# Kernel tuning notes

Measured on AMD Instinct MI355X. Metric: run time of the kernel, lower is better.

Reference implementation:

```python
import jax, jax.numpy as jnp
import numpy as np

C = 16; HP = 16; WP = 16; D = 32; KITER = 4; P = 8; N = P * P; B = 16; HID = 64


def conv2d(x, w, b):
    # x: (B, Cin, H, W), w: (Cout, Cin, kh, kw), 'same' padding for 3x3
    y = jax.lax.conv_general_dilated(x, w, (1, 1), [(1, 1), (1, 1)],
                                     dimension_numbers=('NCHW', 'OIHW', 'NCHW'))
    return y + b[None, :, None, None]


def setup_inputs() -> dict:
    key = jax.random.key(0)
    ks = jax.random.split(key, 20)
    n = lambda k, shape, s=0.1: jax.random.normal(k, shape, jnp.float32) * s
    # 4-neighbor directed grid edges over P x P nodes
    edges = []
    for p in range(P):
        for q in range(P):
            i = p * P + q
            for dp, dq in ((0, 1), (1, 0), (0, -1), (-1, 0)):
                pp, qq = p + dp, q + dq
                if 0 <= pp < P and 0 <= qq < P:
                    edges.append((i, pp * P + qq))
    edge_index = jnp.asarray(np.asarray(edges, np.int32))  # (E, 2) with (i=dst, j=src)
    return {
        'seed': n(ks[0], (B, C, P * HP, P * WP), 1.0),
        'edge_index': edge_index,
        'wq': n(ks[1], (C, D)), 'bq': jnp.zeros((D,), jnp.float32),
        'wk': n(ks[2], (C, D)), 'bk': jnp.zeros((D,), jnp.float32),
        'wm': n(ks[3], (C, C, 3, 3)), 'bm': jnp.zeros((C,), jnp.float32),
        'a_w1': n(ks[4], (2 * D, HID)), 'a_b1': jnp.zeros((HID,), jnp.float32),
        'a_w2': n(ks[5], (HID, HID)), 'a_b2': jnp.zeros((HID,), jnp.float32),
        'a_wo': n(ks[6], (HID, 1)), 'a_bo': jnp.zeros((1,), jnp.float32),
        'g_w': n(ks[7], (C, 1, 3, 3)), 'g_b': jnp.zeros((C,), jnp.float32),
        'gru_wg': n(ks[8], (2 * C, 2 * C, 3, 3)), 'gru_bg': jnp.zeros((2 * C,), jnp.float32),
        'gru_wc': n(ks[9], (C, 2 * C, 3, 3)), 'gru_bc': jnp.zeros((C,), jnp.float32),
    }


def reference(seed, edge_index, wq, bq, wk, bk, wm, bm,
              a_w1, a_b1, a_w2, a_b2, a_wo, a_bo,
              g_w, g_b, gru_wg, gru_bg, gru_wc, gru_bc):
    Bb, Cc, PH, PW = seed.shape
    Pp = PH // HP
    Nn = Pp * Pp
    # patchify: (B,C,PH,PW) -> (B,N,C,H,W), node order is row-major (p,q)
    X = seed.reshape(Bb, Cc, Pp, HP, Pp, WP).transpose(0, 2, 4, 1, 3, 5).reshape(Bb, Nn, Cc, HP, WP)
    ei = edge_index[:, 0]  # dst node i
    ej = edge_index[:, 1]  # src node j
    # GateConv on a spatially-constant map e: conv(e*ones) = e * conv(ones) (+bias).
    ones_map = jnp.ones((1, 1, HP, WP), seed.dtype)
    T = jax.lax.conv_general_dilated(ones_map, g_w, (1, 1), [(1, 1), (1, 1)],
                                     dimension_numbers=('NCHW', 'OIHW', 'NCHW'))  # (1,C,H,W)
    for _ in range(KITER):
        xm = X.mean((-2, -1))  # (B,N,C); mean commutes with the 1x1 convs f_Q/f_K
        q_vec = xm @ wq + bq   # (B,N,d)
        k_vec = xm @ wk + bk
        M = conv2d(X.reshape(Bb * Nn, Cc, HP, WP), wm, bm).reshape(Bb, Nn, Cc, HP, WP)
        # per-edge attention scores via ConcatMLP
        h0 = jnp.concatenate([q_vec[:, ei], k_vec[:, ej]], axis=-1)  # (B,E,2d)
        h1 = jax.nn.relu(h0 @ a_w1 + a_b1)
        h2 = jax.nn.relu(h1 @ a_w2 + a_b2)
        e = (h2 @ a_wo + a_bo)[..., 0]  # (B,E)
        # gate map and gated messages
        G = jax.nn.sigmoid(e[:, :, None, None, None] * T[None] + g_b[None, None, :, None, None])  # (B,E,C,H,W)
        msg = G * M[:, ej]  # gather src patches, gate
        agg = jax.ops.segment_sum(jnp.moveaxis(msg, 1, 0), ei, num_segments=Nn)  # (N,B,C,H,W)
        M_agg = jnp.moveaxis(agg, 0, 1).reshape(Bb * Nn, Cc, HP, WP)
        # ConvGRU cell update
        h = X.reshape(Bb * Nn, Cc, HP, WP)
        zr = jax.nn.sigmoid(conv2d(jnp.concatenate([M_agg, h], axis=1), gru_wg, gru_bg))
        z, r = zr[:, :Cc], zr[:, Cc:]
        cand = jnp.tanh(conv2d(jnp.concatenate([M_agg, r * h], axis=1), gru_wc, gru_bc))
        X = ((1.0 - z) * h + z * cand).reshape(Bb, Nn, Cc, HP, WP)
    # unpatchify
    out = X.reshape(Bb, Pp, Pp, Cc, HP, WP).transpose(0, 3, 1, 4, 2, 5).reshape(Bb, Cc, PH, PW)
    return out
```

## Files before the change

### kernel.cpp

```cpp
#include <hip/hip_runtime.h>
#include <hip/hip_bf16.h>

#define Bt 16
#define Ct 16
#define Nt 64
#define KITERt 4

#define WF_TOTAL 25681
#define SWZ_TOTAL 16384
#define SETUP_IDX (WF_TOTAL + 4096 + Nt + SWZ_TOTAL)
#define SAH_STRIDE 40

typedef __attribute__((ext_vector_type(8))) short bf16x8;
typedef __attribute__((ext_vector_type(4))) short s16x4;
typedef __attribute__((ext_vector_type(4))) float f32x4;

__device__ inline float bf2f(__hip_bfloat16 v) { return __bfloat162float(v); }
__device__ inline short f2bs(float f) {
    __hip_bfloat16 h = __float2bfloat16(f);
    short s; __builtin_memcpy(&s, &h, 2); return s;
}
__device__ inline float bs2f(short s) {
    __hip_bfloat16 h; __builtin_memcpy(&h, &s, 2);
    return __bfloat162float(h);
}
__device__ inline float loadf(const void* p, int i, int isf32) {
    return isf32 ? ((const float*)p)[i]
                 : __bfloat162float(((const __hip_bfloat16*)p)[i]);
}
__device__ inline float sigm(float x) {
    return __builtin_amdgcn_rcpf(1.f + __expf(-x));
}
__device__ inline float tanh_fast(float x) {
    float e = __expf(2.f * x);
    return 1.f - 2.f * __builtin_amdgcn_rcpf(e + 1.f);
}

__global__ __launch_bounds__(256) void setup_kernel(
    const void* __restrict__ seed,
    const void* __restrict__ wq, const void* __restrict__ bq,
    const void* __restrict__ wk, const void* __restrict__ bk,
    const void* __restrict__ wm, const void* __restrict__ bm,
    const void* __restrict__ w1, const void* __restrict__ b1,
    const void* __restrict__ w2, const void* __restrict__ b2,
    const void* __restrict__ wo, const void* __restrict__ bo,
    const void* __restrict__ gw, const void* __restrict__ gb,
    const void* __restrict__ wg, const void* __restrict__ bg,
    const void* __restrict__ wc, const void* __restrict__ bc,
    const int* __restrict__ edge, int E,
    float* __restrict__ Wf, float* __restrict__ Tswz,
    int* __restrict__ counts, int* __restrict__ nbrs,
    __hip_bfloat16* __restrict__ swz,
    short* __restrict__ Xb, float* __restrict__ qv0, float* __restrict__ kv0,
    int* __restrict__ flag)
{
    __shared__ float sred[4];
    __shared__ int sflag;
    __shared__ float xred[64];
    int bn = blockIdx.x, t = threadIdx.x;
    int lane = t & 63, wv = t >> 6;

    {
        float v = fabsf(__bfloat162float(((const __hip_bfloat16*)seed)[t]));
        if (!(v <= 1e30f)) v = 1e30f;
#pragma unroll
        for (int off = 1; off < 64; off <<= 1) v = fmaxf(v, __shfl_xor(v, off, 64));
        if (lane == 0) sred[wv] = v;
        __syncthreads();
        if (t == 0) {
            float m = fmaxf(fmaxf(sred[0], sred[1]), fmaxf(sred[2], sred[3]));
            sflag = (m > 1e10f) ? 1 : 0;
            if (bn == 0) *flag = sflag;
        }
        __syncthreads();
    }
    int isf32 = sflag;

    int idx = bn * 256 + t;
    if (idx < WF_TOTAL) {
        int i = idx;
        const void* base;
        if (i < 512) base = wq;
        else if ((i -= 512) < 32) base = bq;
        else if ((i -= 32) < 512) base = wk;
        else if ((i -= 512) < 32) base = bk;
        else if ((i -= 32) < 2304) base = wm;
        else if ((i -= 2304) < 16) base = bm;
        else if ((i -= 16) < 4096) base = w1;
        else if ((i -= 4096) < 64) base = b1;
        else if ((i -= 64) < 4096) base = w2;
        else if ((i -= 4096) < 64) base = b2;
        else if ((i -= 64) < 64) base = wo;
        else if ((i -= 64) < 1) base = bo;
        else if ((i -= 1) < 16) base = gb;
        else if ((i -= 16) < 9216) base = wg;
        else if ((i -= 9216) < 32) base = bg;
        else if ((i -= 32) < 4608) base = wc;
        else { i -= 4608; base = bc; }
        Wf[idx] = loadf(base, i, isf32);
    } else if (idx < WF_TOTAL + 4096) {
        int j = idx - WF_TOTAL;
        int tt = j >> 4, rr = j & 15;
        int wv2 = tt >> 6, ln = tt & 63, qd = ln >> 4, nn = ln & 15;
        int mt = rr >> 2, r2 = rr & 3;
        int pix = (wv2 * 4 + mt) * 16 + qd * 4 + r2;
        int y = pix >> 4, x = pix & 15;
        float s = 0.f;
        for (int ky = 0; ky < 3; ++ky)
            for (int kx = 0; kx < 3; ++kx) {
                int yy = y + ky - 1, xx = x + kx - 1;
                if (yy >= 0 && yy < 16 && xx >= 0 && xx < 16)
                    s += loadf(gw, nn * 9 + ky * 3 + kx, isf32);
            }
        Tswz[j] = s;
    } else if (idx < WF_TOTAL + 4096 + Nt) {
        int i = idx - WF_TOTAL - 4096;
        int deg = 0;
        for (int e = 0; e < E; ++e)
            if (edge[2 * e] == i && deg < 4) { nbrs[i * 4 + deg] = edge[2 * e + 1]; ++deg; }
        for (int ii = deg; ii < 4; ++ii) nbrs[i * 4 + ii] = 0;
        counts[i] = deg;
    } else if (idx < SETUP_IDX) {
        int j = idx - (WF_TOTAL + 4096 + Nt);
        float val;
        if (j < 9216) {
            int sn = j >> 9, rem = j & 511;
            int ln = rem >> 3, jj = rem & 7;
            int s = sn >> 1, nt = sn & 1;
            int ci = (ln >> 4) * 8 + jj;
            int co = nt * 16 + (ln & 15);
            val = loadf(wg, co * 288 + ci * 9 + s, isf32);
        } else if (j < 9216 + 4608) {
            int j1 = j - 9216;
            int s = j1 >> 9, rem = j1 & 511;
            int ln = rem >> 3, jj = rem & 7;
            int ci = (ln >> 4) * 8 + jj;
            int co = ln & 15;
            val = loadf(wc, co * 288 + ci * 9 + s, isf32);
        } else {
            int j2 = j - 13824;
            int sp = j2 >> 9, rem = j2 & 511;
            int ln = rem >> 3, jj = rem & 7;
            int k = (ln >> 4) * 8 + jj;
            int s = sp * 2 + (k >> 4);
            int ci = k & 15;
            int co = ln & 15;
            val = (s <= 8) ? loadf(wm, co * 144 + ci * 9 + s, isf32) : 0.f;
        }
        swz[j] = __float2bfloat16(val);
    }

    {
        int b = bn >> 6, n = bn & 63;
        int pq = n >> 3, qq = n & 7;
        int y = t >> 4, x = t & 15;
        float v[16];
#pragma unroll
        for (int c = 0; c < 16; ++c)
            v[c] = loadf(seed, ((b * 16 + c) * 128 + pq * 16 + y) * 128 + qq * 16 + x, isf32);
        bf16x8 o0, o1;
#pragma unroll
        for (int c = 0; c < 8; ++c) { o0[c] = f2bs(v[c]); o1[c] = f2bs(v[8 + c]); }
        short* xo = Xb + bn * 4096;
        *(bf16x8*)(xo + t * 16) = o0;
        *(bf16x8*)(xo + t * 16 + 8) = o1;
#pragma unroll
        for (int c = 0; c < 16; ++c) {
            float s = v[c];
#pragma unroll
            for (int off = 1; off < 64; off <<= 1) s += __shfl_xor(s, off, 64);
            if (lane == c) xred[wv * 16 + c] = s;
        }
        __syncthreads();
        if (t < 64) {
            int d = t & 31;
            float a = (t < 32) ? loadf(bq, d, isf32) : loadf(bk, d, isf32);
#pragma unroll
            for (int c = 0; c < 16; ++c) {
                float xm = (xred[c] + xred[16 + c] + xred[32 + c] + xred[48 + c]) * (1.f / 256.f);
                a += xm * ((t < 32) ? loadf(wq, c * 32 + d, isf32)
                                    : loadf(wk, c * 32 + d, isf32));
            }
            if (t < 32) qv0[bn * 32 + d] = a; else kv0[bn * 32 + d] = a;
        }
    }
}

__global__ __launch_bounds__(256) void iter_kernel(
    const short* __restrict__ Xin, short* __restrict__ Xout,
    const float* __restrict__ qin, const float* __restrict__ kin,
    float* __restrict__ qout, float* __restrict__ kout,
    const float* __restrict__ Tswz,
    const short* __restrict__ WmS,
    const short* __restrict__ WgS,
    const short* __restrict__ WcS,
    const float* __restrict__ Wf,
    const int* __restrict__ counts, const int* __restrict__ nbrs,
    const int* __restrict__ flagp, void* __restrict__ out, int last)
{
    __shared__ __align__(16) short sAH[324 * SAH_STRIDE];
    __shared__ float evs[4];
    __shared__ float xred[64];
    int bn = blockIdx.x, b = bn >> 6, i = bn & 63;
    int t = threadIdx.x, lane = t & 63, wv = t >> 6;
    int quad = lane >> 4, n16 = lane & 15;

    int4 nb4 = *(const int4*)(nbrs + i * 4);
    int deg = counts[i];
    int ejl[4] = {nb4.x, nb4.y, nb4.z, nb4.w};
    bf16x8 nbA0, nbA1, nbB0, nbB1;
    if (deg > 0) {
        const short* mp = Xin + (b * 64 + ejl[0]) * 4096 + t * 16;
        nbA0 = *(const bf16x8*)(mp);
        nbA1 = *(const bf16x8*)(mp + 8);
    }

    float T_lane[16];
#pragma unroll
    for (int r = 0; r < 16; ++r) T_lane[r] = Tswz[t * 16 + r];
    float gb_l = Wf[11793 + n16];
    float bm_l = Wf[3392 + n16];

    const short* xown = Xin + bn * 4096;

    for (int p = t; p < 324; p += 256) {
        int yy = p / 18 - 1, xx = p % 18 - 1;
        short* row = sAH + p * SAH_STRIDE;
        if ((unsigned)yy < 16u && (unsigned)xx < 16u) {
            const short* src = xown + (yy * 16 + xx) * 16;
            *(bf16x8*)(row + 16) = *(const bf16x8*)(src);
            *(bf16x8*)(row + 24) = *(const bf16x8*)(src + 8);
        } else {
            bf16x8 z = {0, 0, 0, 0, 0, 0, 0, 0};
            *(bf16x8*)(row) = z;      *(bf16x8*)(row + 8) = z;
            *(bf16x8*)(row + 16) = z; *(bf16x8*)(row + 24) = z;
        }
    }

    if (wv < deg) {
        int ej = ejl[wv];
        float h0 = (lane < 32) ? qin[bn * 32 + lane]
                               : kin[(b * 64 + ej) * 32 + (lane - 32)];
        const float* W1 = Wf + 3408;
        const float* W2 = Wf + 7568;
        float p0 = 0.f, p1 = 0.f, p2 = 0.f, p3 = 0.f;
#pragma unroll
        for (int j = 0; j < 64; j += 4) {
            p0 += __shfl(h0, j + 0, 64) * W1[(j + 0) * 64 + lane];
            p1 += __shfl(h0, j + 1, 64) * W1[(j + 1) * 64 + lane];
            p2 += __shfl(h0, j + 2, 64) * W1[(j + 2) * 64 + lane];
            p3 += __shfl(h0, j + 3, 64) * W1[(j + 3) * 64 + lane];
        }
        float a1 = fmaxf(Wf[7504 + lane] + ((p0 + p1) + (p2 + p3)), 0.f);
        p0 = p1 = p2 = p3 = 0.f;
#pragma unroll
        for (int j = 0; j < 64; j += 4) {
            p0 += __shfl(a1, j + 0, 64) * W2[(j + 0) * 64 + lane];
            p1 += __shfl(a1, j + 1, 64) * W2[(j + 1) * 64 + lane];
            p2 += __shfl(a1, j + 2, 64) * W2[(j + 2) * 64 + lane];
            p3 += __shfl(a1, j + 3, 64) * W2[(j + 3) * 64 + lane];
        }
        float a2 = fmaxf(Wf[11664 + lane] + ((p0 + p1) + (p2 + p3)), 0.f);
        float pe = a2 * Wf[11728 + lane];
#pragma unroll
        for (int off = 32; off; off >>= 1) pe += __shfl_down(pe, off, 64);
        if (lane == 0) evs[wv] = pe + Wf[11792];
    }
    __syncthreads();

    f32x4 magg[4];
#pragma unroll
    for (int mt = 0; mt < 4; ++mt) magg[mt] = (f32x4){0.f, 0.f, 0.f, 0.f};
    int pp = ((t >> 4) + 1) * 18 + (t & 15) + 1;
    for (int ii = 0; ii < deg; ++ii) {
        *(bf16x8*)(sAH + pp * SAH_STRIDE) = nbA0;
        *(bf16x8*)(sAH + pp * SAH_STRIDE + 8) = nbA1;
        if (ii + 1 < deg) {
            const short* mp = Xin + (b * 64 + ejl[ii + 1]) * 4096 + t * 16;
            nbB0 = *(const bf16x8*)(mp);
            nbB1 = *(const bf16x8*)(mp + 8);
        }
        __syncthreads();
        float evv = evs[ii];
        f32x4 acc[4];
#pragma unroll
        for (int mt = 0; mt < 4; ++mt) acc[mt] = (f32x4){bm_l, bm_l, bm_l, bm_l};
#pragma unroll
        for (int sp = 0; sp < 5; ++sp) {
            bf16x8 Bf = *(const bf16x8*)(WmS + sp * 512 + lane * 8);
            int s2 = sp * 2 + (quad >> 1);
            if (s2 > 8) s2 = 8;
            int ky = s2 / 3, kx = s2 - (s2 / 3) * 3;
            int cib = (quad & 1) * 8;
#pragma unroll
            for (int mt = 0; mt < 4; ++mt) {
                int pc = (wv * 4 + mt + ky) * 18 + n16 + kx;
                bf16x8 A = *(const bf16x8*)(sAH + pc * SAH_STRIDE + cib);
                acc[mt] = __builtin_amdgcn_mfma_f32_16x16x32_bf16(A, Bf, acc[mt], 0, 0, 0);
            }
        }
#pragma unroll
        for (int mt = 0; mt < 4; ++mt)
#pragma unroll
            for (int r = 0; r < 4; ++r)
                magg[mt][r] += sigm(evv * T_lane[mt * 4 + r] + gb_l) * acc[mt][r];
        nbA0 = nbB0; nbA1 = nbB1;
        __syncthreads();
    }
#pragma unroll
    for (int mt = 0; mt < 4; ++mt)
#pragma unroll
        for (int r = 0; r < 4; ++r) {
            int p = (wv * 4 + mt + 1) * 18 + quad * 4 + r + 1;
            sAH[p * SAH_STRIDE + n16] = f2bs(magg[mt][r]);
        }
    __syncthreads();

    float bz = Wf[21025 + n16], br = Wf[21025 + 16 + n16];
    f32x4 accZ[4], accR[4];
#pragma unroll
    for (int mt = 0; mt < 4; ++mt) {
        accZ[mt] = (f32x4){bz, bz, bz, bz};
        accR[mt] = (f32x4){br, br, br, br};
    }
#pragma unroll
    for (int s = 0; s < 9; ++s) {
        int ky = s / 3, kx = s - (s / 3) * 3;
        bf16x8 B0 = *(const bf16x8*)(WgS + (s * 2 + 0) * 512 + lane * 8);
        bf16x8 B1 = *(const bf16x8*)(WgS + (s * 2 + 1) * 512 + lane * 8);
#pragma unroll
        for (int mt = 0; mt < 4; ++mt) {
            int pc = (wv * 4 + mt + ky) * 18 + n16 + kx;
            bf16x8 A = *(const bf16x8*)(sAH + pc * SAH_STRIDE + quad * 8);
            accZ[mt] = __builtin_amdgcn_mfma_f32_16x16x32_bf16(A, B0, accZ[mt], 0, 0, 0);
            accR[mt] = __builtin_amdgcn_mfma_f32_16x16x32_bf16(A, B1, accR[mt], 0, 0, 0);
        }
    }
    float zf[16], hf[16], rh[16];
#pragma unroll
    for (int mt = 0; mt < 4; ++mt)
#pragma unroll
        for (int r = 0; r < 4; ++r) {
            int k = mt * 4 + r;
            int ps = (wv * 4 + mt + 1) * 18 + quad * 4 + r + 1;
            hf[k] = bs2f(sAH[ps * SAH_STRIDE + 16 + n16]);
            zf[k] = sigm(accZ[mt][r]);
            rh[k] = sigm(accR[mt][r]) * hf[k];
        }
    __syncthreads();
#pragma unroll
    for (int mt = 0; mt < 4; ++mt)
#pragma unroll
        for (int r = 0; r < 4; ++r) {
            int ps = (wv * 4 + mt + 1) * 18 + quad * 4 + r + 1;
            sAH[ps * SAH_STRIDE + 16 + n16] = f2bs(rh[mt * 4 + r]);
        }
    __syncthreads();

    float bcl = Wf[25665 + n16];
    f32x4 accC[4];
#pragma unroll
    for (int mt = 0; mt < 4; ++mt) accC[mt] = (f32x4){bcl, bcl, bcl, bcl};
#pragma unroll
    for (int s = 0; s < 9; ++s) {
        int ky = s / 3, kx = s - (s / 3) * 3;
        bf16x8 Bc = *(const bf16x8*)(WcS + s * 512 + lane * 8);
#pragma unroll
        for (int mt = 0; mt < 4; ++mt) {
            int pc = (wv * 4 + mt + ky) * 18 + n16 + kx;
            bf16x8 A = *(const bf16x8*)(sAH + pc * SAH_STRIDE + quad * 8);
            accC[mt] = __builtin_amdgcn_mfma_f32_16x16x32_bf16(A, Bc, accC[mt], 0, 0, 0);
        }
    }
    float nxv[16];
#pragma unroll
    for (int mt = 0; mt < 4; ++mt)
#pragma unroll
        for (int r = 0; r < 4; ++r) {
            int k = mt * 4 + r;
            nxv[k] = (1.f - zf[k]) * hf[k] + zf[k] * tanh_fast(accC[mt][r]);
        }

    if (!last) {
        short* xo = Xout + bn * 4096;
        float ssum = 0.f;
#pragma unroll
        for (int mt = 0; mt < 4; ++mt)
#pragma unroll
            for (int r = 0; r < 4; ++r) {
                int k = mt * 4 + r;
                ssum += nxv[k];
                int pix = (wv * 4 + mt) * 16 + quad * 4 + r;
                xo[pix * 16 + n16] = f2bs(nxv[k]);
            }
        ssum += __shfl_xor(ssum, 16, 64);
        ssum += __shfl_xor(ssum, 32, 64);
        if (lane < 16) xred[wv * 16 + lane] = ssum;
        __syncthreads();
        if (t < 64) {
            int d = t & 31;
            const float* W = (t < 32) ? Wf : Wf + 544;
            float a = (t < 32) ? Wf[512 + d] : Wf[1056 + d];
#pragma unroll
            for (int c = 0; c < 16; ++c) {
                float xc = (xred[c] + xred[16 + c] + xred[32 + c] + xred[48 + c]) * (1.f / 256.f);
                a += xc * W[c * 32 + d];
            }
            if (t < 32) qout[bn * 32 + d] = a; else kout[bn * 32 + d] = a;
        }
    } else {
        int isf32 = *flagp;
        int pq = i >> 3, qq = i & 7;
#pragma unroll
        for (int mt = 0; mt < 4; ++mt) {
            long base = ((long)(b * 16 + n16) * 128 + pq * 16 + wv * 4 + mt) * 128
                        + qq * 16 + quad * 4;
            if (isf32) {
                f32x4 v = {nxv[mt * 4], nxv[mt * 4 + 1], nxv[mt * 4 + 2], nxv[mt * 4 + 3]};
                *(f32x4*)((float*)out + base) = v;
            } else {
                s16x4 v = {f2bs(nxv[mt * 4]), f2bs(nxv[mt * 4 + 1]),
                           f2bs(nxv[mt * 4 + 2]), f2bs(nxv[mt * 4 + 3])};
                *(s16x4*)((short*)out + base) = v;
            }
        }
    }
}

extern "C" void kernel_launch(void* const* d_in, const int* in_sizes, int n_in,
                              void* d_out, int out_size, void* d_ws, size_t ws_size,
                              hipStream_t stream)
{
    const void* seed = d_in[0];
    const int* edge = (const int*)d_in[1];
    int E = in_sizes[1] / 2;

    float* ws = (float*)d_ws;
    short* Xb0 = (short*)ws;
    short* Xb1 = (short*)(ws + 2097152);
    float* qv0 = ws + 4194304;
    float* kv0 = qv0 + 32768;
    float* qv1 = kv0 + 32768;
    float* kv1 = qv1 + 32768;
    float* Tswz = kv1 + 32768;
    float* Wf = Tswz + 4096;
    int* nbrs = (int*)(ws + 4355168);
    int* counts = nbrs + 256;
    int* flag = counts + 64;
    __hip_bfloat16* swz = (__hip_bfloat16*)(ws + 4355600);

    const short* WgS = (const short*)swz;
    const short* WcS = (const short*)(swz + 9216);
    const short* WmS = (const short*)(swz + 13824);

    setup_kernel<<<Bt * Nt, 256, 0, stream>>>(
        seed,
        d_in[2], d_in[3], d_in[4], d_in[5], d_in[6], d_in[7], d_in[8], d_in[9],
        d_in[10], d_in[11], d_in[12], d_in[13], d_in[14], d_in[15], d_in[16],
        d_in[17], d_in[18], d_in[19],
        edge, E, Wf, Tswz, counts, nbrs, swz, Xb0, qv0, kv0, flag);

    short* Xs[2] = {Xb0, Xb1};
    float* qs[2] = {qv0, qv1};
    float* ks[2] = {kv0, kv1};
    for (int it = 0; it < KITERt; ++it) {
        int in = it & 1, on = in ^ 1;
        int last = (it == KITERt - 1);
        iter_kernel<<<Bt * Nt, 256, 0, stream>>>(
            Xs[in], Xs[on], qs[in], ks[in], qs[on], ks[on],
            Tswz, WmS, WgS, WcS, Wf, counts, nbrs, flag, d_out, last);
    }
}
```

Baseline: 245.8 us.

## Switch iteration convs to 32x32x16 MFMA with 512-thread blocks

Rewrites the per-patch convolutions in the iteration kernel to use 32x32x16 bf16 MFMA tiles, with 8 waves each covering two pixel rows, and re-swizzles the conv weights and gate template to match. The z and r gates now share one 32-wide accumulator, and the message and candidate convs pad output channels to 32. Neighbour-list construction moves into a single block using direction slots. The goal is fewer MFMA issues and more waves per patch, at the cost of wasted MFMA lanes from channel padding, scalar strided output stores, and extra barriers.

```diff
diff --git a/kernel.cpp b/kernel.cpp
--- a/kernel.cpp
+++ b/kernel.cpp
@@ -7,15 +7,14 @@
 #define KITERt 4
 
 #define WF_TOTAL 25681
-#define SWZ_TOTAL 16384
-#define SETUP_IDX (WF_TOTAL + 4096 + Nt + SWZ_TOTAL)
-#define SAH_STRIDE 40
+#define SWZ_TOTAL 23040
+#define TSWZ_TOTAL 8192
+#define SETUP_IDX (WF_TOTAL + TSWZ_TOTAL + SWZ_TOTAL)
 
 typedef __attribute__((ext_vector_type(8))) short bf16x8;
-typedef __attribute__((ext_vector_type(4))) short s16x4;
 typedef __attribute__((ext_vector_type(4))) float f32x4;
-
-__device__ inline float bf2f(__hip_bfloat16 v) { return __bfloat162float(v); }
+typedef __attribute__((ext_vector_type(16))) float f32x16;
+
 __device__ inline short f2bs(float f) {
     __hip_bfloat16 h = __float2bfloat16(f);
     short s; __builtin_memcpy(&s, &h, 2); return s;
@@ -57,6 +56,7 @@
     __shared__ float sred[4];
     __shared__ int sflag;
     __shared__ float xred[64];
+    __shared__ int snb[256];
     int bn = blockIdx.x, t = threadIdx.x;
     int lane = t & 63, wv = t >> 6;
 
@@ -75,6 +75,30 @@
         __syncthreads();
     }
     int isf32 = sflag;
+
+    if (bn == 0) {
+        if (t < 256) snb[t] = 0;
+        __syncthreads();
+        for (int e = t; e < E; e += 256) {
+            int ei = edge[2 * e], ej = edge[2 * e + 1];
+            int d = ej - ei;
+            int slot = (d == 1) ? 0 : (d == 8) ? 1 : (d == -1) ? 2 : 3;
+            snb[ei * 4 + slot] = ej + 1;
+        }
+        __syncthreads();
+        if (t < 64) {
+            int dcount = 0;
+            int outv[4] = {0, 0, 0, 0};
+#pragma unroll
+            for (int s = 0; s < 4; ++s) {
+                int v = snb[t * 4 + s];
+                if (v) outv[dcount++] = v - 1;
+            }
+            counts[t] = dcount;
+#pragma unroll
+            for (int s = 0; s < 4; ++s) nbrs[t * 4 + s] = outv[s];
+        }
+    }
 
     int idx = bn * 256 + t;
     if (idx < WF_TOTAL) {
@@ -98,54 +122,45 @@
         else if ((i -= 32) < 4608) base = wc;
         else { i -= 4608; base = bc; }
         Wf[idx] = loadf(base, i, isf32);
-    } else if (idx < WF_TOTAL + 4096) {
+    } else if (idx < WF_TOTAL + TSWZ_TOTAL) {
         int j = idx - WF_TOTAL;
-        int tt = j >> 4, rr = j & 15;
-        int wv2 = tt >> 6, ln = tt & 63, qd = ln >> 4, nn = ln & 15;
-        int mt = rr >> 2, r2 = rr & 3;
-        int pix = (wv2 * 4 + mt) * 16 + qd * 4 + r2;
-        int y = pix >> 4, x = pix & 15;
+        int t2 = j >> 4, r = j & 15;
+        int wv2 = t2 >> 6, ln = t2 & 63, n2 = ln & 31, hf2 = ln >> 5;
         float s = 0.f;
-        for (int ky = 0; ky < 3; ++ky)
-            for (int kx = 0; kx < 3; ++kx) {
-                int yy = y + ky - 1, xx = x + kx - 1;
-                if (yy >= 0 && yy < 16 && xx >= 0 && xx < 16)
-                    s += loadf(gw, nn * 9 + ky * 3 + kx, isf32);
-            }
+        if (n2 < 16) {
+            int row = (r & 3) + 8 * (r >> 2) + 4 * hf2;
+            int pix = wv2 * 32 + row;
+            int y = pix >> 4, x = pix & 15;
+            for (int ky = 0; ky < 3; ++ky)
+                for (int kx = 0; kx < 3; ++kx) {
+                    int yy = y + ky - 1, xx = x + kx - 1;
+                    if (yy >= 0 && yy < 16 && xx >= 0 && xx < 16)
+                        s += loadf(gw, n2 * 9 + ky * 3 + kx, isf32);
+                }
+        }
         Tswz[j] = s;
-    } else if (idx < WF_TOTAL + 4096 + Nt) {
-        int i = idx - WF_TOTAL - 4096;
-        int deg = 0;
-        for (int e = 0; e < E; ++e)
-            if (edge[2 * e] == i && deg < 4) { nbrs[i * 4 + deg] = edge[2 * e + 1]; ++deg; }
-        for (int ii = deg; ii < 4; ++ii) nbrs[i * 4 + ii] = 0;
-        counts[i] = deg;
     } else if (idx < SETUP_IDX) {
-        int j = idx - (WF_TOTAL + 4096 + Nt);
+        int j = idx - (WF_TOTAL + TSWZ_TOTAL);
         float val;
         if (j < 9216) {
-            int sn = j >> 9, rem = j & 511;
-            int ln = rem >> 3, jj = rem & 7;
-            int s = sn >> 1, nt = sn & 1;
-            int ci = (ln >> 4) * 8 + jj;
-            int co = nt * 16 + (ln & 15);
-            val = loadf(wg, co * 288 + ci * 9 + s, isf32);
-        } else if (j < 9216 + 4608) {
+            int s = j >> 10, rem = j & 1023;
+            int c = rem >> 9, ln = (rem >> 3) & 63, j8 = rem & 7;
+            int nn = ln & 31, hf2 = ln >> 5;
+            int ci = c * 16 + hf2 * 8 + j8;
+            val = loadf(wg, nn * 288 + ci * 9 + s, isf32);
+        } else if (j < 18432) {
             int j1 = j - 9216;
-            int s = j1 >> 9, rem = j1 & 511;
-            int ln = rem >> 3, jj = rem & 7;
-            int ci = (ln >> 4) * 8 + jj;
-            int co = ln & 15;
-            val = loadf(wc, co * 288 + ci * 9 + s, isf32);
+            int s = j1 >> 10, rem = j1 & 1023;
+            int c = rem >> 9, ln = (rem >> 3) & 63, j8 = rem & 7;
+            int nn = ln & 31, hf2 = ln >> 5;
+            int ci = c * 16 + hf2 * 8 + j8;
+            val = (nn < 16) ? loadf(wc, nn * 288 + ci * 9 + s, isf32) : 0.f;
         } else {
-            int j2 = j - 13824;
-            int sp = j2 >> 9, rem = j2 & 511;
-            int ln = rem >> 3, jj = rem & 7;
-            int k = (ln >> 4) * 8 + jj;
-            int s = sp * 2 + (k >> 4);
-            int ci = k & 15;
-            int co = ln & 15;
-            val = (s <= 8) ? loadf(wm, co * 144 + ci * 9 + s, isf32) : 0.f;
+            int j2 = j - 18432;
+            int s = j2 >> 9, ln = (j2 >> 3) & 63, j8 = j2 & 7;
+            int nn = ln & 31, hf2 = ln >> 5;
+            int ci = hf2 * 8 + j8;
+            val = (nn < 16) ? loadf(wm, nn * 144 + ci * 9 + s, isf32) : 0.f;
         }
         swz[j] = __float2bfloat16(val);
     }
@@ -186,7 +201,7 @@
     }
 }
 
-__global__ __launch_bounds__(256) void iter_kernel(
+__global__ __launch_bounds__(512) void iter_kernel(
     const short* __restrict__ Xin, short* __restrict__ Xout,
     const float* __restrict__ qin, const float* __restrict__ kin,
     float* __restrict__ qout, float* __restrict__ kout,
@@ -198,34 +213,38 @@
     const int* __restrict__ counts, const int* __restrict__ nbrs,
     const int* __restrict__ flagp, void* __restrict__ out, int last)
 {
-    __shared__ __align__(16) short sAH[324 * SAH_STRIDE];
+    __shared__ __align__(16) short sAH[324 * 40];
     __shared__ float evs[4];
-    __shared__ float xred[64];
+    __shared__ float xred[128];
     int bn = blockIdx.x, b = bn >> 6, i = bn & 63;
     int t = threadIdx.x, lane = t & 63, wv = t >> 6;
-    int quad = lane >> 4, n16 = lane & 15;
+    int n = lane & 31, half = lane >> 5;
 
     int4 nb4 = *(const int4*)(nbrs + i * 4);
     int deg = counts[i];
     int ejl[4] = {nb4.x, nb4.y, nb4.z, nb4.w};
-    bf16x8 nbA0, nbA1, nbB0, nbB1;
-    if (deg > 0) {
-        const short* mp = Xin + (b * 64 + ejl[0]) * 4096 + t * 16;
-        nbA0 = *(const bf16x8*)(mp);
-        nbA1 = *(const bf16x8*)(mp + 8);
-    }
+    int hp = t >> 1, ho = (t & 1) * 8;
+    bf16x8 nbA, nbB;
+    if (deg > 0)
+        nbA = *(const bf16x8*)(Xin + (b * 64 + ejl[0]) * 4096 + hp * 16 + ho);
 
     float T_lane[16];
-#pragma unroll
-    for (int r = 0; r < 16; ++r) T_lane[r] = Tswz[t * 16 + r];
-    float gb_l = Wf[11793 + n16];
-    float bm_l = Wf[3392 + n16];
+    {
+        const f32x4* tp = (const f32x4*)(Tswz + t * 16);
+        f32x4 t0 = tp[0], t1 = tp[1], t2 = tp[2], t3 = tp[3];
+#pragma unroll
+        for (int r = 0; r < 4; ++r) {
+            T_lane[r] = t0[r]; T_lane[4 + r] = t1[r];
+            T_lane[8 + r] = t2[r]; T_lane[12 + r] = t3[r];
+        }
+    }
+    float gb_l = Wf[11793 + (n & 15)];
 
     const short* xown = Xin + bn * 4096;
 
-    for (int p = t; p < 324; p += 256) {
-        int yy = p / 18 - 1, xx = p % 18 - 1;
-        short* row = sAH + p * SAH_STRIDE;
+    if (t < 324) {
+        int yy = t / 18 - 1, xx = t % 18 - 1;
+        short* row = sAH + t * 40;
         if ((unsigned)yy < 16u && (unsigned)xx < 16u) {
             const short* src = xown + (yy * 16 + xx) * 16;
             *(bf16x8*)(row + 16) = *(const bf16x8*)(src);
@@ -236,6 +255,8 @@
             *(bf16x8*)(row + 16) = z; *(bf16x8*)(row + 24) = z;
         }
     }
+    int sstage = (((hp >> 4) + 1) * 18 + (hp & 15) + 1) * 40 + ho;
+    if (deg > 0) *(bf16x8*)(sAH + sstage) = nbA;
 
     if (wv < deg) {
         int ej = ejl[wv];
@@ -268,134 +289,119 @@
     }
     __syncthreads();
 
-    f32x4 magg[4];
-#pragma unroll
-    for (int mt = 0; mt < 4; ++mt) magg[mt] = (f32x4){0.f, 0.f, 0.f, 0.f};
-    int pp = ((t >> 4) + 1) * 18 + (t & 15) + 1;
+    const short* Ab = sAH + ((2 * wv + (n >> 4)) * 18 + (n & 15)) * 40 + half * 8;
+
+    float magg[16];
+#pragma unroll
+    for (int r = 0; r < 16; ++r) magg[r] = 0.f;
+    float bm_l = (n < 16) ? Wf[3392 + n] : 0.f;
     for (int ii = 0; ii < deg; ++ii) {
-        *(bf16x8*)(sAH + pp * SAH_STRIDE) = nbA0;
-        *(bf16x8*)(sAH + pp * SAH_STRIDE + 8) = nbA1;
-        if (ii + 1 < deg) {
-            const short* mp = Xin + (b * 64 + ejl[ii + 1]) * 4096 + t * 16;
-            nbB0 = *(const bf16x8*)(mp);
-            nbB1 = *(const bf16x8*)(mp + 8);
-        }
-        __syncthreads();
+        if (ii + 1 < deg)
+            nbB = *(const bf16x8*)(Xin + (b * 64 + ejl[ii + 1]) * 4096 + hp * 16 + ho);
         float evv = evs[ii];
-        f32x4 acc[4];
-#pragma unroll
-        for (int mt = 0; mt < 4; ++mt) acc[mt] = (f32x4){bm_l, bm_l, bm_l, bm_l};
-#pragma unroll
-        for (int sp = 0; sp < 5; ++sp) {
-            bf16x8 Bf = *(const bf16x8*)(WmS + sp * 512 + lane * 8);
-            int s2 = sp * 2 + (quad >> 1);
-            if (s2 > 8) s2 = 8;
-            int ky = s2 / 3, kx = s2 - (s2 / 3) * 3;
-            int cib = (quad & 1) * 8;
-#pragma unroll
-            for (int mt = 0; mt < 4; ++mt) {
-                int pc = (wv * 4 + mt + ky) * 18 + n16 + kx;
-                bf16x8 A = *(const bf16x8*)(sAH + pc * SAH_STRIDE + cib);
-                acc[mt] = __builtin_amdgcn_mfma_f32_16x16x32_bf16(A, Bf, acc[mt], 0, 0, 0);
-            }
-        }
-#pragma unroll
-        for (int mt = 0; mt < 4; ++mt)
-#pragma unroll
-            for (int r = 0; r < 4; ++r)
-                magg[mt][r] += sigm(evv * T_lane[mt * 4 + r] + gb_l) * acc[mt][r];
-        nbA0 = nbB0; nbA1 = nbB1;
-        __syncthreads();
-    }
-#pragma unroll
-    for (int mt = 0; mt < 4; ++mt)
-#pragma unroll
-        for (int r = 0; r < 4; ++r) {
-            int p = (wv * 4 + mt + 1) * 18 + quad * 4 + r + 1;
-            sAH[p * SAH_STRIDE + n16] = f2bs(magg[mt][r]);
-        }
+        f32x16 acc;
+#pragma unroll
+        for (int r = 0; r < 16; ++r) acc[r] = bm_l;
+#pragma unroll
+        for (int s = 0; s < 9; ++s) {
+            int ky = s / 3, kx = s - (s / 3) * 3;
+            bf16x8 Bf = *(const bf16x8*)(WmS + (s * 64 + lane) * 8);
+            bf16x8 A = *(const bf16x8*)(Ab + (ky * 18 + kx) * 40);
+            acc = __builtin_amdgcn_mfma_f32_32x32x16_bf16(A, Bf, acc, 0, 0, 0);
+        }
+#pragma unroll
+        for (int r = 0; r < 16; ++r)
+            magg[r] += sigm(evv * T_lane[r] + gb_l) * acc[r];
+        __syncthreads();
+        if (ii + 1 < deg) *(bf16x8*)(sAH + sstage) = nbB;
+        __syncthreads();
+    }
+    if (n < 16) {
+#pragma unroll
+        for (int r = 0; r < 16; ++r) {
+            int row = (r & 3) + 8 * (r >> 2) + 4 * half;
+            int py = 2 * wv + (row >> 4), px = row & 15;
+            sAH[((py + 1) * 18 + px + 1) * 40 + n] = f2bs(magg[r]);
+        }
+    }
     __syncthreads();
 
-    float bz = Wf[21025 + n16], br = Wf[21025 + 16 + n16];
-    f32x4 accZ[4], accR[4];
-#pragma unroll
-    for (int mt = 0; mt < 4; ++mt) {
-        accZ[mt] = (f32x4){bz, bz, bz, bz};
-        accR[mt] = (f32x4){br, br, br, br};
+    f32x16 azr;
+    {
+        float bg_l = Wf[21025 + n];
+#pragma unroll
+        for (int r = 0; r < 16; ++r) azr[r] = bg_l;
     }
 #pragma unroll
     for (int s = 0; s < 9; ++s) {
         int ky = s / 3, kx = s - (s / 3) * 3;
-        bf16x8 B0 = *(const bf16x8*)(WgS + (s * 2 + 0) * 512 + lane * 8);
-        bf16x8 B1 = *(const bf16x8*)(WgS + (s * 2 + 1) * 512 + lane * 8);
-#pragma unroll
-        for (int mt = 0; mt < 4; ++mt) {
-            int pc = (wv * 4 + mt + ky) * 18 + n16 + kx;
-            bf16x8 A = *(const bf16x8*)(sAH + pc * SAH_STRIDE + quad * 8);
-            accZ[mt] = __builtin_amdgcn_mfma_f32_16x16x32_bf16(A, B0, accZ[mt], 0, 0, 0);
-            accR[mt] = __builtin_amdgcn_mfma_f32_16x16x32_bf16(A, B1, accR[mt], 0, 0, 0);
-        }
-    }
-    float zf[16], hf[16], rh[16];
-#pragma unroll
-    for (int mt = 0; mt < 4; ++mt)
-#pragma unroll
-        for (int r = 0; r < 4; ++r) {
-            int k = mt * 4 + r;
-            int ps = (wv * 4 + mt + 1) * 18 + quad * 4 + r + 1;
-            hf[k] = bs2f(sAH[ps * SAH_STRIDE + 16 + n16]);
-            zf[k] = sigm(accZ[mt][r]);
-            rh[k] = sigm(accR[mt][r]) * hf[k];
-        }
+#pragma unroll
+        for (int c = 0; c < 2; ++c) {
+            bf16x8 Bf = *(const bf16x8*)(WgS + ((s * 2 + c) * 64 + lane) * 8);
+            bf16x8 A = *(const bf16x8*)(Ab + (ky * 18 + kx) * 40 + c * 16);
+            azr = __builtin_amdgcn_mfma_f32_32x32x16_bf16(A, Bf, azr, 0, 0, 0);
+        }
+    }
+    float hf[16], zf[16];
+#pragma unroll
+    for (int r = 0; r < 16; ++r) {
+        int row = (r & 3) + 8 * (r >> 2) + 4 * half;
+        int py = 2 * wv + (row >> 4), px = row & 15;
+        hf[r] = bs2f(sAH[((py + 1) * 18 + px + 1) * 40 + 16 + (n & 15)]);
+    }
     __syncthreads();
-#pragma unroll
-    for (int mt = 0; mt < 4; ++mt)
-#pragma unroll
-        for (int r = 0; r < 4; ++r) {
-            int ps = (wv * 4 + mt + 1) * 18 + quad * 4 + r + 1;
-            sAH[ps * SAH_STRIDE + 16 + n16] = f2bs(rh[mt * 4 + r]);
-        }
+    if (n >= 16) {
+#pragma unroll
+        for (int r = 0; r < 16; ++r) {
+            int row = (r & 3) + 8 * (r >> 2) + 4 * half;
+            int py = 2 * wv + (row >> 4), px = row & 15;
+            sAH[((py + 1) * 18 + px + 1) * 40 + 16 + (n & 15)] =
+                f2bs(sigm(azr[r]) * hf[r]);
+        }
+    } else {
+#pragma unroll
+        for (int r = 0; r < 16; ++r) zf[r] = sigm(azr[r]);
+    }
     __syncthreads();
 
-    float bcl = Wf[25665 + n16];
-    f32x4 accC[4];
-#pragma unroll
-    for (int mt = 0; mt < 4; ++mt) accC[mt] = (f32x4){bcl, bcl, bcl, bcl};
+    f32x16 acd;
+    {
+        float bc_l = (n < 16) ? Wf[25665 + n] : 0.f;
+#pragma unroll
+        for (int r = 0; r < 16; ++r) acd[r] = bc_l;
+    }
 #pragma unroll
     for (int s = 0; s < 9; ++s) {
         int ky = s / 3, kx = s - (s / 3) * 3;
-        bf16x8 Bc = *(const bf16x8*)(WcS + s * 512 + lane * 8);
-#pragma unroll
-        for (int mt = 0; mt < 4; ++mt) {
-            int pc = (wv * 4 + mt + ky) * 18 + n16 + kx;
-            bf16x8 A = *(const bf16x8*)(sAH + pc * SAH_STRIDE + quad * 8);
-            accC[mt] = __builtin_amdgcn_mfma_f32_16x16x32_bf16(A, Bc, accC[mt], 0, 0, 0);
-        }
-    }
-    float nxv[16];
-#pragma unroll
-    for (int mt = 0; mt < 4; ++mt)
-#pragma unroll
-        for (int r = 0; r < 4; ++r) {
-            int k = mt * 4 + r;
-            nxv[k] = (1.f - zf[k]) * hf[k] + zf[k] * tanh_fast(accC[mt][r]);
-        }
-
+#pragma unroll
+        for (int c = 0; c < 2; ++c) {
+            bf16x8 Bf = *(const bf16x8*)(WcS + ((s * 2 + c) * 64 + lane) * 8);
+            bf16x8 A = *(const bf16x8*)(Ab + (ky * 18 + kx) * 40 + c * 16);
+            acd = __builtin_amdgcn_mfma_f32_32x32x16_bf16(A, Bf, acd, 0, 0, 0);
+        }
+    }
+    if (n < 16) {
+        float ssum = 0.f;
+        int isf32 = *flagp;
+        int pq = i >> 3, qq = i & 7;
+#pragma unroll
+        for (int r = 0; r < 16; ++r) {
+            int row = (r & 3) + 8 * (r >> 2) + 4 * half;
+            int py = 2 * wv + (row >> 4), px = row & 15;
+            float nx = (1.f - zf[r]) * hf[r] + zf[r] * tanh_fast(acd[r]);
+            ssum += nx;
+            if (!last) {
+                Xout[bn * 4096 + (py * 16 + px) * 16 + n] = f2bs(nx);
+            } else {
+                long base = ((long)(b * 16 + n) * 128 + pq * 16 + py) * 128 + qq * 16 + px;
+                if (isf32) ((float*)out)[base] = nx;
+                else ((short*)out)[base] = f2bs(nx);
+            }
+        }
+        ssum += __shfl_xor(ssum, 32, 64);
+        if (lane < 16) xred[wv * 16 + n] = ssum;
+    }
     if (!last) {
-        short* xo = Xout + bn * 4096;
-        float ssum = 0.f;
-#pragma unroll
-        for (int mt = 0; mt < 4; ++mt)
-#pragma unroll
-            for (int r = 0; r < 4; ++r) {
-                int k = mt * 4 + r;
-                ssum += nxv[k];
-                int pix = (wv * 4 + mt) * 16 + quad * 4 + r;
-                xo[pix * 16 + n16] = f2bs(nxv[k]);
-            }
-        ssum += __shfl_xor(ssum, 16, 64);
-        ssum += __shfl_xor(ssum, 32, 64);
-        if (lane < 16) xred[wv * 16 + lane] = ssum;
         __syncthreads();
         if (t < 64) {
             int d = t & 31;
@@ -403,26 +409,12 @@
             float a = (t < 32) ? Wf[512 + d] : Wf[1056 + d];
 #pragma unroll
             for (int c = 0; c < 16; ++c) {
-                float xc = (xred[c] + xred[16 + c] + xred[32 + c] + xred[48 + c]) * (1.f / 256.f);
-                a += xc * W[c * 32 + d];
+                float xc = 0.f;
+#pragma unroll
+                for (int w = 0; w < 8; ++w) xc += xred[w * 16 + c];
+                a += xc * (1.f / 256.f) * W[c * 32 + d];
             }
             if (t < 32) qout[bn * 32 + d] = a; else kout[bn * 32 + d] = a;
-        }
-    } else {
-        int isf32 = *flagp;
-        int pq = i >> 3, qq = i & 7;
-#pragma unroll
-        for (int mt = 0; mt < 4; ++mt) {
-            long base = ((long)(b * 16 + n16) * 128 + pq * 16 + wv * 4 + mt) * 128
-                        + qq * 16 + quad * 4;
-            if (isf32) {
-                f32x4 v = {nxv[mt * 4], nxv[mt * 4 + 1], nxv[mt * 4 + 2], nxv[mt * 4 + 3]};
-                *(f32x4*)((float*)out + base) = v;
-            } else {
-                s16x4 v = {f2bs(nxv[mt * 4]), f2bs(nxv[mt * 4 + 1]),
-                           f2bs(nxv[mt * 4 + 2]), f2bs(nxv[mt * 4 + 3])};
-                *(s16x4*)((short*)out + base) = v;
-            }
         }
     }
 }
@@ -442,16 +434,16 @@
     float* kv0 = qv0 + 32768;
     float* qv1 = kv0 + 32768;
     float* kv1 = qv1 + 32768;
-    float* Tswz = kv1 + 32768;
-    float* Wf = Tswz + 4096;
-    int* nbrs = (int*)(ws + 4355168);
+    float* Tswz = ws + 4325376;
+    float* Wf = ws + 4333568;
+    int* nbrs = (int*)(ws + 4360000);
     int* counts = nbrs + 256;
     int* flag = counts + 64;
-    __hip_bfloat16* swz = (__hip_bfloat16*)(ws + 4355600);
+    __hip_bfloat16* swz = (__hip_bfloat16*)(ws + 4360400);
 
     const short* WgS = (const short*)swz;
     const short* WcS = (const short*)(swz + 9216);
-    const short* WmS = (const short*)(swz + 13824);
+    const short* WmS = (const short*)(swz + 18432);
 
     setup_kernel<<<Bt * Nt, 256, 0, stream>>>(
         seed,
@@ -466,7 +458,7 @@
     for (int it = 0; it < KITERt; ++it) {
         int in = it & 1, on = in ^ 1;
         int last = (it == KITERt - 1);
-        iter_kernel<<<Bt * Nt, 256, 0, stream>>>(
+        iter_kernel<<<Bt * Nt, 512, 0, stream>>>(
             Xs[in], Xs[on], qs[in], ks[in], qs[on], ks[on],
             Tswz, WmS, WgS, WcS, Wf, counts, nbrs, flag, d_out, last);
     }
```

Measured after the change: 323.0 us. +31.4%, slower.

## Double-buffer neighbor patches in LDS and drop extra GRU barriers

Applied to the files above, without the earlier changes.

Adds a second LDS buffer (sNB) so neighbor patches alternate between the sAH channel slot and sNB. This removes one __syncthreads per neighbor iteration, since the next patch is written after the compute. The r*h product is written into sNB instead of overwriting h in sAH, which drops a barrier and a register array before the candidate conv. The edge-to-neighbor table is now built in parallel by block 0 through shared memory instead of each thread scanning every edge. The cost is more LDS use, which may lower occupancy, and slot-ordered neighbors that assume a grid topology.

```diff
diff --git a/kernel.cpp b/kernel.cpp
--- a/kernel.cpp
+++ b/kernel.cpp
@@ -10,12 +10,12 @@
 #define SWZ_TOTAL 16384
 #define SETUP_IDX (WF_TOTAL + 4096 + Nt + SWZ_TOTAL)
 #define SAH_STRIDE 40
+#define SNB_STRIDE 20
 
 typedef __attribute__((ext_vector_type(8))) short bf16x8;
 typedef __attribute__((ext_vector_type(4))) short s16x4;
 typedef __attribute__((ext_vector_type(4))) float f32x4;
 
-__device__ inline float bf2f(__hip_bfloat16 v) { return __bfloat162float(v); }
 __device__ inline short f2bs(float f) {
     __hip_bfloat16 h = __float2bfloat16(f);
     short s; __builtin_memcpy(&s, &h, 2); return s;
@@ -57,6 +57,7 @@
     __shared__ float sred[4];
     __shared__ int sflag;
     __shared__ float xred[64];
+    __shared__ int snb[256];
     int bn = blockIdx.x, t = threadIdx.x;
     int lane = t & 63, wv = t >> 6;
 
@@ -75,6 +76,30 @@
         __syncthreads();
     }
     int isf32 = sflag;
+
+    if (bn == 0) {
+        snb[t] = 0;
+        __syncthreads();
+        for (int e = t; e < E; e += 256) {
+            int ei = edge[2 * e], ej = edge[2 * e + 1];
+            int d = ej - ei;
+            int slot = (d == 1) ? 0 : (d == 8) ? 1 : (d == -1) ? 2 : 3;
+            snb[ei * 4 + slot] = ej + 1;
+        }
+        __syncthreads();
+        if (t < 64) {
+            int dcount = 0;
+            int outv[4] = {0, 0, 0, 0};
+#pragma unroll
+            for (int s = 0; s < 4; ++s) {
+                int v = snb[t * 4 + s];
+                if (v) outv[dcount++] = v - 1;
+            }
+            counts[t] = dcount;
+#pragma unroll
+            for (int s = 0; s < 4; ++s) nbrs[t * 4 + s] = outv[s];
+        }
+    }
 
     int idx = bn * 256 + t;
     if (idx < WF_TOTAL) {
@@ -113,14 +138,7 @@
                     s += loadf(gw, nn * 9 + ky * 3 + kx, isf32);
             }
         Tswz[j] = s;
-    } else if (idx < WF_TOTAL + 4096 + Nt) {
-        int i = idx - WF_TOTAL - 4096;
-        int deg = 0;
-        for (int e = 0; e < E; ++e)
-            if (edge[2 * e] == i && deg < 4) { nbrs[i * 4 + deg] = edge[2 * e + 1]; ++deg; }
-        for (int ii = deg; ii < 4; ++ii) nbrs[i * 4 + ii] = 0;
-        counts[i] = deg;
-    } else if (idx < SETUP_IDX) {
+    } else if (idx < SETUP_IDX && idx >= WF_TOTAL + 4096 + Nt) {
         int j = idx - (WF_TOTAL + 4096 + Nt);
         float val;
         if (j < 9216) {
@@ -199,6 +217,7 @@
     const int* __restrict__ flagp, void* __restrict__ out, int last)
 {
     __shared__ __align__(16) short sAH[324 * SAH_STRIDE];
+    __shared__ __align__(16) short sNB[324 * SNB_STRIDE];
     __shared__ float evs[4];
     __shared__ float xred[64];
     int bn = blockIdx.x, b = bn >> 6, i = bn & 63;
@@ -214,6 +233,10 @@
         nbA0 = *(const bf16x8*)(mp);
         nbA1 = *(const bf16x8*)(mp + 8);
     }
+    float h0 = 0.f;
+    if (wv < deg)
+        h0 = (lane < 32) ? qin[bn * 32 + lane]
+                         : kin[(b * 64 + ejl[wv]) * 32 + (lane - 32)];
 
     float T_lane[16];
 #pragma unroll
@@ -222,6 +245,7 @@
     float bm_l = Wf[3392 + n16];
 
     const short* xown = Xin + bn * 4096;
+    int pp = ((t >> 4) + 1) * 18 + (t & 15) + 1;
 
     for (int p = t; p < 324; p += 256) {
         int yy = p / 18 - 1, xx = p % 18 - 1;
@@ -234,13 +258,16 @@
             bf16x8 z = {0, 0, 0, 0, 0, 0, 0, 0};
             *(bf16x8*)(row) = z;      *(bf16x8*)(row + 8) = z;
             *(bf16x8*)(row + 16) = z; *(bf16x8*)(row + 24) = z;
-        }
+            short* row2 = sNB + p * SNB_STRIDE;
+            *(bf16x8*)(row2) = z;     *(bf16x8*)(row2 + 8) = z;
+        }
+    }
+    if (deg > 0) {
+        *(bf16x8*)(sAH + pp * SAH_STRIDE) = nbA0;
+        *(bf16x8*)(sAH + pp * SAH_STRIDE + 8) = nbA1;
     }
 
     if (wv < deg) {
-        int ej = ejl[wv];
-        float h0 = (lane < 32) ? qin[bn * 32 + lane]
-                               : kin[(b * 64 + ej) * 32 + (lane - 32)];
         const float* W1 = Wf + 3408;
         const float* W2 = Wf + 7568;
         float p0 = 0.f, p1 = 0.f, p2 = 0.f, p3 = 0.f;
@@ -271,16 +298,14 @@
     f32x4 magg[4];
 #pragma unroll
     for (int mt = 0; mt < 4; ++mt) magg[mt] = (f32x4){0.f, 0.f, 0.f, 0.f};
-    int pp = ((t >> 4) + 1) * 18 + (t & 15) + 1;
     for (int ii = 0; ii < deg; ++ii) {
-        *(bf16x8*)(sAH + pp * SAH_STRIDE) = nbA0;
-        *(bf16x8*)(sAH + pp * SAH_STRIDE + 8) = nbA1;
         if (ii + 1 < deg) {
             const short* mp = Xin + (b * 64 + ejl[ii + 1]) * 4096 + t * 16;
             nbB0 = *(const bf16x8*)(mp);
             nbB1 = *(const bf16x8*)(mp + 8);
         }
-        __syncthreads();
+        const short* nbase = (ii & 1) ? sNB : sAH;
+        int nstride = (ii & 1) ? SNB_STRIDE : SAH_STRIDE;
         float evv = evs[ii];
         f32x4 acc[4];
 #pragma unroll
@@ -295,7 +320,7 @@
 #pragma unroll
             for (int mt = 0; mt < 4; ++mt) {
                 int pc = (wv * 4 + mt + ky) * 18 + n16 + kx;
-                bf16x8 A = *(const bf16x8*)(sAH + pc * SAH_STRIDE + cib);
+                bf16x8 A = *(const bf16x8*)(nbase + pc * nstride + cib);
                 acc[mt] = __builtin_amdgcn_mfma_f32_16x16x32_bf16(A, Bf, acc[mt], 0, 0, 0);
             }
         }
@@ -304,7 +329,12 @@
 #pragma unroll
             for (int r = 0; r < 4; ++r)
                 magg[mt][r] += sigm(evv * T_lane[mt * 4 + r] + gb_l) * acc[mt][r];
-        nbA0 = nbB0; nbA1 = nbB1;
+        if (ii + 1 < deg) {
+            short* sb = ((ii + 1) & 1) ? sNB : sAH;
+            int ss = ((ii + 1) & 1) ? SNB_STRIDE : SAH_STRIDE;
+            *(bf16x8*)(sb + pp * ss) = nbB0;
+            *(bf16x8*)(sb + pp * ss + 8) = nbB1;
+        }
         __syncthreads();
     }
 #pragma unroll
@@ -336,7 +366,7 @@
             accR[mt] = __builtin_amdgcn_mfma_f32_16x16x32_bf16(A, B1, accR[mt], 0, 0, 0);
         }
     }
-    float zf[16], hf[16], rh[16];
+    float zf[16], hf[16];
 #pragma unroll
     for (int mt = 0; mt < 4; ++mt)
 #pragma unroll
@@ -345,18 +375,13 @@
             int ps = (wv * 4 + mt + 1) * 18 + quad * 4 + r + 1;
             hf[k] = bs2f(sAH[ps * SAH_STRIDE + 16 + n16]);
             zf[k] = sigm(accZ[mt][r]);
-            rh[k] = sigm(accR[mt][r]) * hf[k];
+            sNB[ps * SNB_STRIDE + n16] = f2bs(sigm(accR[mt][r]) * hf[k]);
         }
     __syncthreads();
-#pragma unroll
-    for (int mt = 0; mt < 4; ++mt)
-#pragma unroll
-        for (int r = 0; r < 4; ++r) {
-            int ps = (wv * 4 + mt + 1) * 18 + quad * 4 + r + 1;
-            sAH[ps * SAH_STRIDE + 16 + n16] = f2bs(rh[mt * 4 + r]);
-        }
-    __syncthreads();
-
+
+    const short* cbase = (quad < 2) ? sAH : sNB;
+    int cstride = (quad < 2) ? SAH_STRIDE : SNB_STRIDE;
+    int coff = (quad < 2) ? quad * 8 : (quad - 2) * 8;
     float bcl = Wf[25665 + n16];
     f32x4 accC[4];
 #pragma unroll
@@ -368,7 +393,7 @@
 #pragma unroll
         for (int mt = 0; mt < 4; ++mt) {
             int pc = (wv * 4 + mt + ky) * 18 + n16 + kx;
-            bf16x8 A = *(const bf16x8*)(sAH + pc * SAH_STRIDE + quad * 8);
+            bf16x8 A = *(const bf16x8*)(cbase + pc * cstride + coff);
             accC[mt] = __builtin_amdgcn_mfma_f32_16x16x32_bf16(A, Bc, accC[mt], 0, 0, 0);
         }
     }
```

Result: slower. 398.7 us (+62.2%).
